# Kernel tuning notes

Hardware: AMD Instinct MI355X
Metric: run time of the kernel (lower is better)

## Reference

```python
import jax, jax.numpy as jnp
import numpy as np

# NOTE: submodules (VecLayerNorm, VecLinear, VecActivation, VNAttention,
# VNCrossAttention, VNDynamicGraphAttention) are not in the provided source;
# they are reconstructed per standard Vector-Neuron (VN) equivariant layers.

B, C, NQ, NV, K, HEADS = 2, 128, 2048, 2048, 16, 8
HID = 4 * C
EPS = 1e-6
NS = 0.2  # LeakyReLU(0.2) slope used by VecActivation


def vec_layernorm(x, gamma, beta):
    # x: [B,C,3,N] -- equivariant LN: normalize per-channel vector norms,
    # LayerNorm the norms over the channel dim, rescale directions.
    n = jnp.sqrt(jnp.sum(x * x, axis=2, keepdims=True) + EPS)  # [B,C,1,N]
    mu = jnp.mean(n, axis=1, keepdims=True)
    var = jnp.var(n, axis=1, keepdims=True)
    ln = (n - mu) / jnp.sqrt(var + EPS) * gamma[None, :, None, None] + beta[None, :, None, None]
    return x / (n + EPS) * ln


def vlin(x, W):
    # VecLinear: bias-free linear over channel dim (equivariance). x: [B,C,3,N]
    return jnp.einsum('oc,bctn->botn', W, x)


def vn_attention(xq, xkv, Wq, Wk, Wv, Wo):
    # Global equivariant multi-head attention; scores from 3D-vector inner products.
    Bq, Cc, _, Nq = xq.shape
    Dh = Cc // HEADS
    q = vlin(xq, Wq).reshape(Bq, HEADS, Dh, 3, Nq)
    k = vlin(xkv, Wk).reshape(Bq, HEADS, Dh, 3, -1)
    vv = vlin(xkv, Wv).reshape(Bq, HEADS, Dh, 3, -1)
    s = jnp.einsum('bhdtn,bhdtm->bhnm', q, k) / np.float32(np.sqrt(3 * Dh))
    a = jax.nn.softmax(s, axis=-1)
    o = jnp.einsum('bhnm,bhdtm->bhdtn', a, vv).reshape(Bq, Cc, 3, Nq)
    return vlin(o, Wo)


def graph_attention(xq, xv, idx, We):
    # Local kNN graph attention: gather neighbor features by idx, build edge
    # features concat(v_j - q_i, q_i) -> VecLinear, softmax-weight over k neighbors.
    Bq, Cc, _, Nq = xq.shape
    vt = jnp.transpose(xv, (0, 3, 2, 1))                 # [B,Nv,3,C]
    nbr = jax.vmap(lambda vb, ib: vb[ib])(vt, idx)       # [B,Nq,k,3,C]
    qt = jnp.transpose(xq, (0, 3, 2, 1))                 # [B,Nq,3,C]
    center = qt[:, :, None, :, :]
    edge = jnp.concatenate([nbr - center, jnp.broadcast_to(center, nbr.shape)], axis=-1)  # [B,Nq,k,3,2C]
    feat = jnp.einsum('oc,bnktc->bnkto', We, edge)        # [B,Nq,k,3,C]
    s = jnp.einsum('bntc,bnktc->bnk', qt, nbr) / np.float32(np.sqrt(3 * Cc))
    a = jax.nn.softmax(s, axis=-1)
    out = jnp.einsum('bnk,bnkto->bnto', a, feat)          # [B,Nq,3,C]
    return jnp.transpose(out, (0, 3, 2, 1))               # [B,C,3,Nq]


def vn_leaky(x, D):
    # VN-LeakyReLU: learned direction d = D x; reflect negative half-space.
    d = vlin(x, D)
    dot = jnp.sum(x * d, axis=2, keepdims=True)
    dsq = jnp.sum(d * d, axis=2, keepdims=True)
    xneg = x - (dot / (dsq + EPS)) * d
    return NS * x + (1.0 - NS) * jnp.where(dot >= 0, x, xneg)


def setup_inputs() -> dict:
    key = jax.random.key(0)
    ks = jax.random.split(key, 24)

    def w(k_, o, i):
        return jax.random.normal(k_, (o, i), jnp.float32) / np.float32(np.sqrt(i))

    inp = {
        'q': jax.random.normal(ks[0], (B, C, 3, NQ), jnp.float32),
        'v': jax.random.normal(ks[1], (B, C, 3, NV), jnp.float32),
        'q_pos': jax.random.normal(ks[2], (B, NQ, 3), jnp.float32),
        'v_pos': jax.random.normal(ks[3], (B, NV, 3), jnp.float32),
        'self_attn_idx': jax.random.randint(ks[4], (B, NQ, K), 0, NQ),
        'cross_attn_idx': jax.random.randint(ks[5], (B, NQ, K), 0, NV),
        # VecLayerNorm affine params (norm1, norm2, norm_q, norm_v)
        'g1': jnp.ones((C,), jnp.float32), 'b1': jnp.zeros((C,), jnp.float32),
        'g2': jnp.ones((C,), jnp.float32), 'b2': jnp.zeros((C,), jnp.float32),
        'gq': jnp.ones((C,), jnp.float32), 'bq': jnp.zeros((C,), jnp.float32),
        'gv': jnp.ones((C,), jnp.float32), 'bv': jnp.zeros((C,), jnp.float32),
        # self attention (global VN attn + local graph attn + concat merge)
        'Wq_s': w(ks[6], C, C), 'Wk_s': w(ks[7], C, C), 'Wv_s': w(ks[8], C, C), 'Wo_s': w(ks[9], C, C),
        'We_s': w(ks[10], C, 2 * C), 'Wm_s': w(ks[11], C, 2 * C),
        # cross attention
        'Wq_c': w(ks[12], C, C), 'Wk_c': w(ks[13], C, C), 'Wv_c': w(ks[14], C, C), 'Wo_c': w(ks[15], C, C),
        'We_c': w(ks[16], C, 2 * C), 'Wm_c': w(ks[17], C, 2 * C),
        # MLP: VecLinear(C->4C) -> VN-LeakyReLU -> VecLinear(4C->C)
        'W1': w(ks[18], HID, C), 'Dact': w(ks[19], HID, HID), 'W2': w(ks[20], C, HID),
    }
    return inp


def reference(q, v, q_pos, v_pos, self_attn_idx, cross_attn_idx,
              g1, b1, g2, b2, gq, bq, gv, bv,
              Wq_s, Wk_s, Wv_s, Wo_s, We_s, Wm_s,
              Wq_c, Wk_c, Wv_c, Wo_c, We_c, Wm_c,
              W1, Dact, W2):
    # --- self-attention block (norm1 -> global attn + kNN graph attn -> merge -> residual)
    nx = vec_layernorm(q, g1, b1)
    f1 = vn_attention(nx, nx, Wq_s, Wk_s, Wv_s, Wo_s)
    f2 = graph_attention(nx, nx, self_attn_idx, We_s)
    q = q + vlin(jnp.concatenate([f1, f2], axis=1), Wm_s)
    # --- cross-attention block (norm_q / norm_v -> global cross attn + kNN cross graph attn -> merge -> residual)
    nq = vec_layernorm(q, gq, bq)
    nv = vec_layernorm(v, gv, bv)
    f1 = vn_attention(nq, nv, Wq_c, Wk_c, Wv_c, Wo_c)
    f2 = graph_attention(nq, nv, cross_attn_idx, We_c)
    q = q + vlin(jnp.concatenate([f1, f2], axis=1), Wm_c)
    # --- equivariant MLP (norm2 -> VecLinear -> VN-LeakyReLU -> VecLinear -> residual)
    nx = vec_layernorm(q, g2, b2)
    h = vn_leaky(vlin(nx, W1), Dact)
    q = q + vlin(h, W2)
    return q
```

## Files before the change

kernel.cpp:

```cpp
#include <hip/hip_runtime.h>
#include <math.h>

#define B_    2
#define C_    128
#define N_    2048
#define HID_  512
#define HEADS_ 8
#define EPS_  1e-6f
#define NS_   0.2f
#define KSPLIT 8

typedef __attribute__((ext_vector_type(8))) short short8v;
typedef __attribute__((ext_vector_type(4))) float f32x4;
typedef unsigned short ush;
typedef unsigned int u32;

__device__ inline ush f2bf(float f) {
    unsigned u = __float_as_uint(f);
    u += 0x7FFF + ((u >> 16) & 1);
    return (ush)(u >> 16);
}
__device__ inline float bf2f(ush u) { return __uint_as_float((u32)u << 16); }

__device__ inline u32 splitpack(float x) {
    ush hi = f2bf(x);
    float hf = __uint_as_float((u32)hi << 16);
    ush lo = f2bf(x - hf);
    return ((u32)hi << 16) | (u32)lo;
}

__device__ inline void unpack_hi(const u32* buf, short8v& h0, short8v& h1) {
    ush h[16];
    #pragma unroll
    for (int j = 0; j < 16; ++j) h[j] = (ush)(buf[j] >> 16);
    h0 = *(short8v*)&h[0]; h1 = *(short8v*)&h[8];
}

struct LNArgs {
    const float* x[2]; const float* g[2]; const float* bt[2]; ush* ysp[2];
};
__global__ __launch_bounds__(256) void ln_kernel(LNArgs a)
{
    __shared__ float norms[128][32];
    __shared__ float red1[8][32];
    __shared__ float red2[8][32];
    const int s = blockIdx.z;
    const float* x = a.x[s];
    const float* gma = a.g[s];
    const float* bta = a.bt[s];
    ush* ysp = a.ysp[s];

    const int b  = blockIdx.y;
    const int n0 = blockIdx.x * 32;
    const int nn = threadIdx.x & 31;
    const int cg = threadIdx.x >> 5;

    float s1 = 0.f, s2 = 0.f;
    for (int it = 0; it < 16; ++it) {
        int c = it * 8 + cg;
        size_t base = ((size_t)(b * C_ + c) * 3) * N_ + n0 + nn;
        float x0 = x[base], x1 = x[base + N_], x2 = x[base + 2 * N_];
        float nr = sqrtf(x0 * x0 + x1 * x1 + x2 * x2 + EPS_);
        norms[c][nn] = nr;
        s1 += nr; s2 += nr * nr;
    }
    red1[cg][nn] = s1; red2[cg][nn] = s2;
    __syncthreads();
    float S1 = 0.f, S2 = 0.f;
    #pragma unroll
    for (int g = 0; g < 8; ++g) { S1 += red1[g][nn]; S2 += red2[g][nn]; }
    float mu   = S1 * (1.f / 128.f);
    float var  = S2 * (1.f / 128.f) - mu * mu;
    float rstd = rsqrtf(var + EPS_);

    for (int it = 0; it < 16; ++it) {
        int c = it * 8 + cg;
        float nr = norms[c][nn];
        float ln = (nr - mu) * rstd * gma[c] + bta[c];
        float sc = ln / (nr + EPS_);
        size_t base = ((size_t)(b * C_ + c) * 3) * N_ + n0 + nn;
        ysp[base]          = f2bf(x[base] * sc);
        ysp[base + N_]     = f2bf(x[base + N_] * sc);
        ysp[base + 2 * N_] = f2bf(x[base + 2 * N_] * sc);
    }
}

struct WCArgs { const float* src[9]; u32* dst[9]; int n[9]; float scale[9]; };
__global__ __launch_bounds__(256) void wconv_kernel(WCArgs a)
{
    const int w = blockIdx.y;
    const int i = blockIdx.x * 256 + threadIdx.x;
    if (i < a.n[w]) a.dst[w][i] = splitpack(a.src[w][i] * a.scale[w]);
}

struct WFArgs {
    const float* Wm[2]; const float* Wo[2]; const float* We[2];
    u32* Wfa[2]; u32* Wfb[2];
};
__global__ __launch_bounds__(256) void wfuse_kernel(WFArgs a)
{
    const int tg = blockIdx.x * 256 + threadIdx.x;
    const int p = tg / 49152;
    const int rem = tg % 49152;
    if (rem < 16384) {
        const int o = rem >> 7, k = rem & 127;
        const float* Wm = a.Wm[p];
        const float* Wo = a.Wo[p];
        float acc = 0.f;
        #pragma unroll 4
        for (int c = 0; c < 128; ++c)
            acc += Wm[o * 256 + c] * Wo[c * 128 + k];
        a.Wfa[p][o * 128 + k] = splitpack(acc);
    } else {
        const int r2 = rem - 16384;
        const int o = r2 >> 8, k = r2 & 255;
        const float* Wm = a.Wm[p];
        const float* We = a.We[p];
        float acc = 0.f;
        #pragma unroll 4
        for (int c = 0; c < 128; ++c)
            acc += Wm[o * 256 + 128 + c] * We[c * 256 + k];
        a.Wfb[p][o * 256 + k] = splitpack(acc);
    }
}

template <int XMODE, int OMODE, bool XBF>
__device__ __forceinline__ void gemm_tile(
    const u32* __restrict__ Wsp, int wstride,
    const void* __restrict__ Xv, int K,
    const float* __restrict__ Z, float* __restrict__ Y,
    ush* __restrict__ Ybf, ush* __restrict__ Ytr,
    int b, int m0, int o0loc, int oglob, int Ostr,
    ush (*Wh)[64], ush (*Xh)[64])
{
    const int M = 3 * N_;
    const int tid = threadIdx.x;
    const int lane = tid & 63, wv = tid >> 6;
    const int col = lane & 15, grp = lane >> 4;
    const int wo = wv >> 1, wm = wv & 1;

    f32x4 acc[2][2];
    #pragma unroll
    for (int i = 0; i < 2; ++i)
        #pragma unroll
        for (int j = 0; j < 2; ++j) { f32x4 z = {0.f,0.f,0.f,0.f}; acc[i][j] = z; }

    for (int kk = 0; kk < K; kk += 64) {
        {
            const int o = tid >> 2, kg = tid & 3;
            const u32* src = Wsp + (size_t)(o0loc + o) * wstride + kk + kg * 16;
            u32 buf[16];
            #pragma unroll
            for (int j = 0; j < 4; ++j) *(uint4*)&buf[j * 4] = *(const uint4*)(src + j * 4);
            const int s0 = ((kg * 2)     ^ (o & 7)) << 3;
            const int s1 = ((kg * 2 + 1) ^ (o & 7)) << 3;
            short8v h0, h1; unpack_hi(buf, h0, h1);
            *(short8v*)&Wh[o][s0] = h0; *(short8v*)&Wh[o][s1] = h1;
        }
        if (XMODE == 0) {
            const int m = lane, kq = wv;
            const int s0 = ((kq * 2)     ^ (m & 7)) << 3;
            const int s1 = ((kq * 2 + 1) ^ (m & 7)) << 3;
            if (XBF) {
                const ush* src = (const ush*)Xv + ((size_t)b * K + kk + kq * 16) * M + m0 + m;
                ush h[16];
                #pragma unroll
                for (int j = 0; j < 16; ++j) h[j] = src[(size_t)j * M];
                *(short8v*)&Xh[m][s0] = *(short8v*)&h[0];
                *(short8v*)&Xh[m][s1] = *(short8v*)&h[8];
            } else {
                const u32* src = (const u32*)Xv + ((size_t)b * K + kk + kq * 16) * M + m0 + m;
                u32 buf[16];
                #pragma unroll
                for (int j = 0; j < 16; ++j) buf[j] = src[(size_t)j * M];
                short8v h0, h1; unpack_hi(buf, h0, h1);
                *(short8v*)&Xh[m][s0] = h0; *(short8v*)&Xh[m][s1] = h1;
            }
        } else {
            const int m = tid >> 2, kg = tid & 3;
            const int mg = m0 + m;
            const int n = mg & (N_ - 1), t = mg >> 11;
            const int s0 = ((kg * 2)     ^ (m & 7)) << 3;
            const int s1 = ((kg * 2 + 1) ^ (m & 7)) << 3;
            const ush* src = (const ush*)Xv + ((size_t)(b * N_ + n) * 3 + t) * K + kk + kg * 16;
            ush h[16];
            *(uint4*)&h[0] = *(const uint4*)(src);
            *(uint4*)&h[8] = *(const uint4*)(src + 8);
            *(short8v*)&Xh[m][s0] = *(short8v*)&h[0];
            *(short8v*)&Xh[m][s1] = *(short8v*)&h[8];
        }
        __syncthreads();
        #pragma unroll
        for (int kc = 0; kc < 2; ++kc) {
            const int sk = ((kc * 4 + grp) ^ (col & 7)) << 3;
            short8v ah0 = *(const short8v*)&Wh[wo * 32 + col][sk];
            short8v ah1 = *(const short8v*)&Wh[wo * 32 + 16 + col][sk];
            short8v xh0 = *(const short8v*)&Xh[wm * 32 + col][sk];
            short8v xh1 = *(const short8v*)&Xh[wm * 32 + 16 + col][sk];
            acc[0][0] = __builtin_amdgcn_mfma_f32_16x16x32_bf16(ah0, xh0, acc[0][0], 0, 0, 0);
            acc[0][1] = __builtin_amdgcn_mfma_f32_16x16x32_bf16(ah0, xh1, acc[0][1], 0, 0, 0);
            acc[1][0] = __builtin_amdgcn_mfma_f32_16x16x32_bf16(ah1, xh0, acc[1][0], 0, 0, 0);
            acc[1][1] = __builtin_amdgcn_mfma_f32_16x16x32_bf16(ah1, xh1, acc[1][1], 0, 0, 0);
        }
        __syncthreads();
    }
    #pragma unroll
    for (int of = 0; of < 2; ++of) {
        #pragma unroll
        for (int r = 0; r < 4; ++r) {
            const int o = oglob + wo * 32 + of * 16 + grp * 4 + r;
            #pragma unroll
            for (int mf = 0; mf < 2; ++mf) {
                const int mloc = m0 + wm * 32 + mf * 16 + col;
                const size_t idx = ((size_t)b * Ostr + o) * M + mloc;
                float v = acc[of][mf][r];
                if (OMODE == 0) {
                    if (Z) v += Z[idx];
                    Y[idx] = v;
                }
                if (OMODE == 3) Ybf[idx] = f2bf(v);
                if (OMODE == 4) {
                    ush bv = f2bf(v);
                    const int t = mloc >> 11, n = mloc & (N_ - 1);
                    const int h = (o >> 4) & 7, cl = o & 15;
                    const int d = cl * 3 + t;
                    if (o >= 256) {
                        const int kt = n >> 6, hh = (n >> 5) & 1, db = d >> 4;
                        const size_t idx2 = ((size_t)(b * 8 + h) * 192
                                           + (kt * 2 + hh) * 3 + db) * 512
                                          + (((n >> 3) & 3) * 16 + (d & 15)) * 8 + (n & 7);
                        Ybf[idx2] = bv;
                    } else {
                        const int isK = (o >> 7) & 1;
                        const int qg = n >> 4, half = d >> 5;
                        const size_t idx2 = ((size_t)(isK * 16 + b * 8 + h) * 256
                                           + qg * 2 + half) * 512
                                          + (((d >> 3) & 3) * 16 + (n & 15)) * 8 + (d & 7);
                        Ytr[idx2] = bv;
                    }
                }
            }
        }
    }
}

template <int XMODE, int OMODE, bool XBF>
__global__ __launch_bounds__(256) void gemm_kernel2(
    const u32* __restrict__ Wsp, int wstride,
    const void* __restrict__ Xv,
    const float* __restrict__ Z,
    float* __restrict__ Y, ush* __restrict__ Ybf,
    int Ostr, int obase, int K)
{
    __shared__ __align__(16) ush Wh[64][64];
    __shared__ __align__(16) ush Xh[64][64];
    gemm_tile<XMODE, OMODE, XBF>(Wsp, wstride, Xv, K, Z, Y, Ybf, nullptr,
                            blockIdx.z, blockIdx.x * 64,
                            blockIdx.y * 64, obase + blockIdx.y * 64, Ostr,
                            Wh, Xh);
}

__global__ __launch_bounds__(256) void wm2_kernel(
    const u32* __restrict__ Wfa, const u32* __restrict__ Wfb,
    const ush* __restrict__ ao, const ush* __restrict__ gb,
    const float* __restrict__ Z, float* __restrict__ Y)
{
    __shared__ __align__(16) ush Wh[64][64];
    __shared__ __align__(16) ush Xh[64][64];
    const int M = 3 * N_;
    const int b = blockIdx.z;
    const int m0 = blockIdx.x * 64;
    const int o0 = blockIdx.y * 64;
    const int tid = threadIdx.x;
    const int lane = tid & 63, wv = tid >> 6;
    const int col = lane & 15, grp = lane >> 4;
    const int wo = wv >> 1, wm = wv & 1;

    f32x4 acc[2][2];
    #pragma unroll
    for (int i = 0; i < 2; ++i)
        #pragma unroll
        for (int j = 0; j < 2; ++j) { f32x4 z = {0.f,0.f,0.f,0.f}; acc[i][j] = z; }

    for (int kk = 0; kk < 128; kk += 64) {
        {
            const int o = tid >> 2, kg = tid & 3;
            const u32* src = Wfa + (size_t)(o0 + o) * 128 + kk + kg * 16;
            u32 buf[16];
            #pragma unroll
            for (int j = 0; j < 4; ++j) *(uint4*)&buf[j * 4] = *(const uint4*)(src + j * 4);
            const int s0 = ((kg * 2)     ^ (o & 7)) << 3;
            const int s1 = ((kg * 2 + 1) ^ (o & 7)) << 3;
            short8v h0, h1; unpack_hi(buf, h0, h1);
            *(short8v*)&Wh[o][s0] = h0; *(short8v*)&Wh[o][s1] = h1;
        }
        {
            const int m = lane, kq = wv;
            const int s0 = ((kq * 2)     ^ (m & 7)) << 3;
            const int s1 = ((kq * 2 + 1) ^ (m & 7)) << 3;
            const ush* src = ao + ((size_t)b * 128 + kk + kq * 16) * M + m0 + m;
            ush h[16];
            #pragma unroll
            for (int j = 0; j < 16; ++j) h[j] = src[(size_t)j * M];
            *(short8v*)&Xh[m][s0] = *(short8v*)&h[0];
            *(short8v*)&Xh[m][s1] = *(short8v*)&h[8];
        }
        __syncthreads();
        #pragma unroll
        for (int kc = 0; kc < 2; ++kc) {
            const int sk = ((kc * 4 + grp) ^ (col & 7)) << 3;
            short8v ah0 = *(const short8v*)&Wh[wo * 32 + col][sk];
            short8v ah1 = *(const short8v*)&Wh[wo * 32 + 16 + col][sk];
            short8v xh0 = *(const short8v*)&Xh[wm * 32 + col][sk];
            short8v xh1 = *(const short8v*)&Xh[wm * 32 + 16 + col][sk];
            acc[0][0] = __builtin_amdgcn_mfma_f32_16x16x32_bf16(ah0, xh0, acc[0][0], 0, 0, 0);
            acc[0][1] = __builtin_amdgcn_mfma_f32_16x16x32_bf16(ah0, xh1, acc[0][1], 0, 0, 0);
            acc[1][0] = __builtin_amdgcn_mfma_f32_16x16x32_bf16(ah1, xh0, acc[1][0], 0, 0, 0);
            acc[1][1] = __builtin_amdgcn_mfma_f32_16x16x32_bf16(ah1, xh1, acc[1][1], 0, 0, 0);
        }
        __syncthreads();
    }

    for (int kk = 0; kk < 256; kk += 64) {
        {
            const int o = tid >> 2, kg = tid & 3;
            const u32* src = Wfb + (size_t)(o0 + o) * 256 + kk + kg * 16;
            u32 buf[16];
            #pragma unroll
            for (int j = 0; j < 4; ++j) *(uint4*)&buf[j * 4] = *(const uint4*)(src + j * 4);
            const int s0 = ((kg * 2)     ^ (o & 7)) << 3;
            const int s1 = ((kg * 2 + 1) ^ (o & 7)) << 3;
            short8v h0, h1; unpack_hi(buf, h0, h1);
            *(short8v*)&Wh[o][s0] = h0; *(short8v*)&Wh[o][s1] = h1;
        }
        {
            const int m = tid >> 2, kg = tid & 3;
            const int mg = m0 + m;
            const int n = mg & (N_ - 1), t = mg >> 11;
            const int s0 = ((kg * 2)     ^ (m & 7)) << 3;
            const int s1 = ((kg * 2 + 1) ^ (m & 7)) << 3;
            const ush* src = gb + ((size_t)(b * N_ + n) * 3 + t) * 256 + kk + kg * 16;
            ush h[16];
            *(uint4*)&h[0] = *(const uint4*)(src);
            *(uint4*)&h[8] = *(const uint4*)(src + 8);
            *(short8v*)&Xh[m][s0] = *(short8v*)&h[0];
            *(short8v*)&Xh[m][s1] = *(short8v*)&h[8];
        }
        __syncthreads();
        #pragma unroll
        for (int kc = 0; kc < 2; ++kc) {
            const int sk = ((kc * 4 + grp) ^ (col & 7)) << 3;
            short8v ah0 = *(const short8v*)&Wh[wo * 32 + col][sk];
            short8v ah1 = *(const short8v*)&Wh[wo * 32 + 16 + col][sk];
            short8v xh0 = *(const short8v*)&Xh[wm * 32 + col][sk];
            short8v xh1 = *(const short8v*)&Xh[wm * 32 + 16 + col][sk];
            acc[0][0] = __builtin_amdgcn_mfma_f32_16x16x32_bf16(ah0, xh0, acc[0][0], 0, 0, 0);
            acc[0][1] = __builtin_amdgcn_mfma_f32_16x16x32_bf16(ah0, xh1, acc[0][1], 0, 0, 0);
            acc[1][0] = __builtin_amdgcn_mfma_f32_16x16x32_bf16(ah1, xh0, acc[1][0], 0, 0, 0);
            acc[1][1] = __builtin_amdgcn_mfma_f32_16x16x32_bf16(ah1, xh1, acc[1][1], 0, 0, 0);
        }
        __syncthreads();
    }

    #pragma unroll
    for (int of = 0; of < 2; ++of) {
        #pragma unroll
        for (int r = 0; r < 4; ++r) {
            const int o = o0 + wo * 32 + of * 16 + grp * 4 + r;
            #pragma unroll
            for (int mf = 0; mf < 2; ++mf) {
                const int mloc = m0 + wm * 32 + mf * 16 + col;
                const size_t idx = ((size_t)b * 128 + o) * M + mloc;
                Y[idx] = acc[of][mf][r] + Z[idx];
            }
        }
    }
}

struct QKVArgs {
    const u32* W0; const u32* W1; const u32* W2;
    const ush* X0; const ush* X1; const ush* X2;
};

__global__ __launch_bounds__(256) void qkv_tr_kernel(QKVArgs A,
        ush* __restrict__ vfm, ush* __restrict__ qktb,
        const ush* __restrict__ ts0, ush* __restrict__ td0,
        const ush* __restrict__ ts1, ush* __restrict__ td1)
{
    __shared__ __align__(16) ush Wh[64][64];
    __shared__ __align__(16) ush Xh[64][64];
    __shared__ ush ttile[32][34];
    const int bx = blockIdx.x;
    if (bx < 1152) {
        const int z = bx / 576, rem = bx % 576;
        const int y = rem / 96, x = rem % 96;
        const int wi = y >> 1;
        const u32* W = wi == 0 ? A.W0 : (wi == 1 ? A.W1 : A.W2);
        const ush* X = wi == 0 ? A.X0 : (wi == 1 ? A.X1 : A.X2);
        gemm_tile<0, 4, true>(W, 128, X, 128, nullptr, nullptr, vfm, qktb,
                        z, x * 64, (y & 1) * 64, y * 64, 384,
                        Wh, Xh);
    } else {
        int i = bx - 1152;
        const int which = i / 1536; i %= 1536;
        const ush* src = which ? ts1 : ts0;
        ush* dst = which ? td1 : td0;
        const int x = i & 63, y = (i >> 6) & 3, z = i >> 8;
        const int b = z / 3, t = z % 3;
        const int n0 = x * 32, c0 = y * 32;
        const int tx = threadIdx.x & 31, ty = threadIdx.x >> 5;
        #pragma unroll
        for (int p = 0; p < 4; ++p) {
            int c = c0 + ty + p * 8;
            ttile[ty + p * 8][tx] = src[((size_t)(b * C_ + c) * 3 + t) * N_ + n0 + tx];
        }
        __syncthreads();
        #pragma unroll
        for (int p = 0; p < 4; ++p) {
            int n = n0 + ty + p * 8;
            dst[((size_t)(b * N_ + n) * 3 + t) * C_ + c0 + tx] = ttile[tx][ty + p * 8];
        }
    }
}

__global__ __launch_bounds__(256) void attn_mfma_kernel(
    const ush* __restrict__ vfm, const ush* __restrict__ qktb,
    ush* __restrict__ pacc, float* __restrict__ pml)
{
    __shared__ __align__(16) ush Pl[4][2][16][64];

    const int flat = blockIdx.x;
    const int xcd  = flat & 7;
    const int slot = flat >> 3;
    const int gid  = xcd * 4 + (slot >> 6);
    const int q32  = slot & 63;
    const int bh   = gid & 15;
    const int zz   = gid >> 4;

    const int tid = threadIdx.x;
    const int lane = tid & 63, wv = tid >> 6;
    const int col = lane & 15, grp = lane >> 4;
    const int c7  = col & 7;
    const int kz  = zz * 4 + wv;
    const int ks0 = kz * (N_ / KSPLIT);

    const ush* Qpl = qktb + (size_t)bh * 131072;
    const ush* Kpl = qktb + (size_t)(16 + bh) * 131072;
    const ush* Vpl = vfm  + (size_t)bh * 98304;

    short8v qf[2][2];
    #pragma unroll
    for (int qi = 0; qi < 2; ++qi) {
        const int qg = q32 * 2 + qi;
        qf[qi][0] = *(const short8v*)(Qpl + ((size_t)qg * 2 + 0) * 512 + lane * 8);
        qf[qi][1] = *(const short8v*)(Qpl + ((size_t)qg * 2 + 1) * 512 + lane * 8);
    }

    f32x4 acc[2][3];
    #pragma unroll
    for (int qi = 0; qi < 2; ++qi)
        #pragma unroll
        for (int db = 0; db < 3; ++db) { f32x4 z = {0.f,0.f,0.f,0.f}; acc[qi][db] = z; }
    float m_i[2] = {0.f, 0.f};
    float l_l[2] = {0.f, 0.f};

    const int NT = (N_ / KSPLIT) / 64;
    for (int mt = 0; mt < NT; ++mt) {
        const int m0 = ks0 + mt * 64;

        short8v ka[4][2];
        #pragma unroll
        for (int kb = 0; kb < 4; ++kb) {
            const size_t kg = (m0 >> 4) + kb;
            ka[kb][0] = *(const short8v*)(Kpl + (kg * 2 + 0) * 512 + lane * 8);
            ka[kb][1] = *(const short8v*)(Kpl + (kg * 2 + 1) * 512 + lane * 8);
        }
        const int kt = m0 >> 6;
        short8v vf[2][3];
        #pragma unroll
        for (int hh = 0; hh < 2; ++hh)
            #pragma unroll
            for (int db = 0; db < 3; ++db)
                vf[hh][db] = *(const short8v*)(Vpl + (size_t)((kt * 2 + hh) * 3 + db) * 512 + lane * 8);

        f32x4 sf[2][4];
        __builtin_amdgcn_s_setprio(1);
        #pragma unroll
        for (int qi = 0; qi < 2; ++qi)
            #pragma unroll
            for (int kb = 0; kb < 4; ++kb) {
                f32x4 z = {0.f, 0.f, 0.f, 0.f};
                z = __builtin_amdgcn_mfma_f32_16x16x32_bf16(ka[kb][0], qf[qi][0], z, 0, 0, 0);
                z = __builtin_amdgcn_mfma_f32_16x16x32_bf16(ka[kb][1], qf[qi][1], z, 0, 0, 0);
                sf[qi][kb] = z;
            }
        __builtin_amdgcn_s_setprio(0);

        #pragma unroll
        for (int qi = 0; qi < 2; ++qi) {
            float psum = 0.f;
            #pragma unroll
            for (int kb = 0; kb < 4; ++kb) {
                float e0 = __expf(sf[qi][kb][0] - m_i[qi]);
                float e1 = __expf(sf[qi][kb][1] - m_i[qi]);
                float e2 = __expf(sf[qi][kb][2] - m_i[qi]);
                float e3 = __expf(sf[qi][kb][3] - m_i[qi]);
                psum += (e0 + e1) + (e2 + e3);
                u32 r0, r1;
                asm("v_cvt_pk_bf16_f32 %0, %1, %2" : "=v"(r0) : "v"(e0), "v"(e1));
                asm("v_cvt_pk_bf16_f32 %0, %1, %2" : "=v"(r1) : "v"(e2), "v"(e3));
                const int un = (4 * kb + grp) ^ (c7 << 1);
                uint2 pk2; pk2.x = r0; pk2.y = r1;
                *(uint2*)&Pl[wv][qi][col][un << 2] = pk2;
            }
            l_l[qi] += psum;
        }

        __builtin_amdgcn_s_setprio(1);
        #pragma unroll
        for (int qi = 0; qi < 2; ++qi)
            #pragma unroll
            for (int hh = 0; hh < 2; ++hh) {
                const int ur = (8 * hh + 2 * grp) ^ (c7 << 1);
                short8v pf = *(const short8v*)&Pl[wv][qi][col][ur << 2];
                #pragma unroll
                for (int db = 0; db < 3; ++db)
                    acc[qi][db] = __builtin_amdgcn_mfma_f32_16x16x32_bf16(vf[hh][db], pf, acc[qi][db], 0, 0, 0);
            }
        __builtin_amdgcn_s_setprio(0);

        #pragma unroll
        for (int qi = 0; qi < 2; ++qi) {
            float pmax = -1e30f;
            #pragma unroll
            for (int kb = 0; kb < 4; ++kb)
                #pragma unroll
                for (int r = 0; r < 4; ++r) pmax = fmaxf(pmax, sf[qi][kb][r]);
            pmax = fmaxf(pmax, __shfl_xor(pmax, 16, 64));
            pmax = fmaxf(pmax, __shfl_xor(pmax, 32, 64));
            if (!__all(pmax - m_i[qi] <= 8.0f)) {
                float mnew = fmaxf(m_i[qi], pmax);
                float sc = __expf(m_i[qi] - mnew);
                l_l[qi] *= sc;
                #pragma unroll
                for (int db = 0; db < 3; ++db) {
                    acc[qi][db][0] *= sc; acc[qi][db][1] *= sc;
                    acc[qi][db][2] *= sc; acc[qi][db][3] *= sc;
                }
                m_i[qi] = mnew;
            }
        }
    }

    const int ntile = q32 >> 1, qh = q32 & 1;
    const size_t pb = (size_t)(kz * 16 + bh) * 32 + ntile;
    #pragma unroll
    for (int qi = 0; qi < 2; ++qi) {
        float l = l_l[qi];
        l += __shfl_xor(l, 16, 64);
        l += __shfl_xor(l, 32, 64);
        const int q = qh * 32 + qi * 16 + col;
        #pragma unroll
        for (int db = 0; db < 3; ++db)
            #pragma unroll
            for (int r = 0; r < 4; ++r) {
                int d = db * 16 + grp * 4 + r;
                pacc[pb * 3072 + d * 64 + q] = f2bf(acc[qi][db][r]);
            }
        if (grp == 0) {
            pml[pb * 128 + q]      = m_i[qi];
            pml[pb * 128 + 64 + q] = l;
        }
    }
}

__global__ __launch_bounds__(256) void reduce_graph_kernel(
    const ush* __restrict__ pacc, const float* __restrict__ pml,
    ush* __restrict__ ao,
    const ush* __restrict__ tq, const ush* __restrict__ tv,
    const int* __restrict__ idx, ush* __restrict__ gbuf)
{
    __shared__ float centerf[384];
    __shared__ ush nbr_l[16][384];
    __shared__ float sd[16];
    __shared__ int nbr_i[16];
    const int tid = threadIdx.x;

    if (blockIdx.x < 512) {
        const int nt = blockIdx.x & 31, bh = blockIdx.x >> 5;
        const int b = bh >> 3, h = bh & 7;
        const int q = tid & 63, dg = tid >> 6;

        size_t pb[KSPLIT];
        float m[KSPLIT], l[KSPLIT];
        #pragma unroll
        for (int kz = 0; kz < KSPLIT; ++kz) {
            pb[kz] = (size_t)(kz * 16 + bh) * 32 + nt;
            m[kz] = pml[pb[kz] * 128 + q];
            l[kz] = pml[pb[kz] * 128 + 64 + q];
        }
        float ms = -1e30f;
        #pragma unroll
        for (int kz = 0; kz < KSPLIT; ++kz) ms = fmaxf(ms, m[kz]);
        float w[KSPLIT], ls = 0.f;
        #pragma unroll
        for (int kz = 0; kz < KSPLIT; ++kz) { w[kz] = __expf(m[kz] - ms); ls += l[kz] * w[kz]; }
        const float inv = 1.f / ls;

        const size_t hb = ((size_t)(b * C_ + h * 16)) * 3 * N_;
        #pragma unroll
        for (int j = 0; j < 12; ++j) {
            int d = dg * 12 + j;
            float o = 0.f;
            #pragma unroll
            for (int kz = 0; kz < KSPLIT; ++kz)
                o += bf2f(pacc[pb[kz] * 3072 + d * 64 + q]) * w[kz];
            ao[hb + (size_t)d * N_ + nt * 64 + q] = f2bf(o * inv);
        }
    } else {
        const int j = blockIdx.x - 512;
        const int b = j >> 11, n = j & 2047;
        const ush* qrow = tq + (size_t)(b * N_ + n) * 384;
        for (int e = tid; e < 384; e += 256) centerf[e] = bf2f(qrow[e]);
        if (tid < 16) nbr_i[tid] = idx[(size_t)(b * N_ + n) * 16 + tid];
        __syncthreads();

        const int lane = tid & 63, wv = tid >> 6;
        for (int kk = 0; kk < 4; ++kk) {
            int k = wv * 4 + kk;
            const u32* vrow = (const u32*)(tv + ((size_t)b * N_ + nbr_i[k]) * 384);
            float p = 0.f;
            #pragma unroll
            for (int jj = 0; jj < 3; ++jj) {
                int e2 = lane + jj * 64;
                u32 v2 = vrow[e2];
                ((u32*)nbr_l[k])[e2] = v2;
                p += centerf[e2 * 2]     * bf2f((ush)(v2 & 0xffff))
                   + centerf[e2 * 2 + 1] * bf2f((ush)(v2 >> 16));
            }
            #pragma unroll
            for (int off = 32; off; off >>= 1) p += __shfl_down(p, off, 64);
            if (lane == 0) sd[k] = p * 0.05103103630798288f;
        }
        __syncthreads();

        float mx = -1e30f;
        #pragma unroll
        for (int k = 0; k < 16; ++k) mx = fmaxf(mx, sd[k]);
        float a[16]; float ssum = 0.f;
        #pragma unroll
        for (int k = 0; k < 16; ++k) { a[k] = __expf(sd[k] - mx); ssum += a[k]; }
        float inv = 1.f / ssum;

        for (int e = tid; e < 384; e += 256) {
            float accv = 0.f;
            #pragma unroll
            for (int k = 0; k < 16; ++k)
                accv += a[k] * bf2f(nbr_l[k][e]);
            accv *= inv;
            float ce = centerf[e];
            int t = e >> 7, c = e & 127;
            size_t gb = ((size_t)(b * N_ + n) * 3 + t) * 256;
            gbuf[gb + c]       = f2bf(accv - ce);
            gbuf[gb + 128 + c] = f2bf(ce);
        }
    }
}

__global__ __launch_bounds__(256) void leaky_kernel(const ush* __restrict__ x,
                                                    const ush* __restrict__ d,
                                                    ush* __restrict__ y)
{
    size_t p = (size_t)blockIdx.x * 256 + threadIdx.x;
    size_t bh = p / N_, n = p % N_;
    size_t base = bh * 3 * N_ + n;
    float x0 = bf2f(x[base]), x1 = bf2f(x[base + N_]), x2 = bf2f(x[base + 2 * N_]);
    float d0 = bf2f(d[base]), d1 = bf2f(d[base + N_]), d2 = bf2f(d[base + 2 * N_]);
    float dot = x0 * d0 + x1 * d1 + x2 * d2;
    float dsq = d0 * d0 + d1 * d1 + d2 * d2;
    float f = dot / (dsq + EPS_);
    bool pos = dot >= 0.f;
    float y0 = pos ? x0 : x0 - f * d0;
    float y1 = pos ? x1 : x1 - f * d1;
    float y2 = pos ? x2 : x2 - f * d2;
    y[base]          = f2bf(NS_ * x0 + (1.f - NS_) * y0);
    y[base + N_]     = f2bf(NS_ * x1 + (1.f - NS_) * y1);
    y[base + 2 * N_] = f2bf(NS_ * x2 + (1.f - NS_) * y2);
}

extern "C" void kernel_launch(void* const* d_in, const int* in_sizes, int n_in,
                              void* d_out, int out_size, void* d_ws, size_t ws_size,
                              hipStream_t stream)
{
    const float* q_in = (const float*)d_in[0];
    const float* v_in = (const float*)d_in[1];
    const int*   idx_s = (const int*)d_in[4];
    const int*   idx_c = (const int*)d_in[5];
    const float* g1 = (const float*)d_in[6];
    const float* b1 = (const float*)d_in[7];
    const float* g2 = (const float*)d_in[8];
    const float* b2 = (const float*)d_in[9];
    const float* gq = (const float*)d_in[10];
    const float* bq = (const float*)d_in[11];
    const float* gv = (const float*)d_in[12];
    const float* bv = (const float*)d_in[13];
    float* out = (float*)d_out;
    float* ws  = (float*)d_ws;

    const size_t S1 = (size_t)B_ * C_ * 3 * N_;
    ush*   gbuf_b= (ush*)(ws);
    ush*   nx_b  = (ush*)(ws + 2*S1);
    ush*   nv_b  = (ush*)(ws + 3*S1);
    ush*   vfm   = (ush*)(ws + 4*S1);
    ush*   qktb  = (ush*)(ws + 5*S1) + S1;
    ush*   ao_b  = (ush*)(ws + 7*S1);
    float* qa    = ws + 12*S1;
    float* qb    = ws + 13*S1;
    ush*   t1_b  = (ush*)(ws + 14*S1);
    ush*   t2_b  = (ush*)(ws + 15*S1);
    u32*   wsp   = (u32*)(ws + 16*S1);
    ush*   pacc  = (ush*)(ws + 8*S1);
    float* pml   = (float*)(ws + 2*S1);
    ush*   hd_b  = (ush*)(ws + 1*S1);
    ush*   h1_b  = (ush*)(ws + 14*S1);
    ush*   h1_b2 = (ush*)(ws + 8*S1);

    const int wn[9]   = {16384,16384,16384, 16384,16384,16384, 65536,262144,65536};
    const int wsrc[9] = {14,15,16, 20,21,22, 26,27,28};
    u32* wd[9];
    {
        int off = 0;
        for (int i = 0; i < 9; ++i) { wd[i] = wsp + off; off += wn[i]; }
    }
    u32 *Wq_s = wd[0], *Wk_s = wd[1], *Wv_s = wd[2];
    u32 *Wq_c = wd[3], *Wk_c = wd[4], *Wv_c = wd[5];
    u32 *W1 = wd[6], *Dact = wd[7], *W2 = wd[8];
    u32* Wfa_s = wsp + 491520;
    u32* Wfb_s = Wfa_s + 16384;
    u32* Wfa_c = Wfb_s + 32768;
    u32* Wfb_c = Wfa_c + 16384;

    hipMemsetAsync(qktb, 0, (size_t)32 * 131072 * sizeof(ush), stream);

    {
        WCArgs a;
        for (int i = 0; i < 9; ++i) {
            a.src[i] = (const float*)d_in[wsrc[i]];
            a.dst[i] = wd[i];
            a.n[i]   = wn[i];
            a.scale[i] = 1.f;
        }
        a.scale[0] = 0.14433756729740643f;
        a.scale[3] = 0.14433756729740643f;
        wconv_kernel<<<dim3(1024, 9), 256, 0, stream>>>(a);
    }
    {
        WFArgs a;
        a.Wm[0] = (const float*)d_in[19]; a.Wo[0] = (const float*)d_in[17]; a.We[0] = (const float*)d_in[18];
        a.Wm[1] = (const float*)d_in[25]; a.Wo[1] = (const float*)d_in[23]; a.We[1] = (const float*)d_in[24];
        a.Wfa[0] = Wfa_s; a.Wfb[0] = Wfb_s;
        a.Wfa[1] = Wfa_c; a.Wfb[1] = Wfb_c;
        wfuse_kernel<<<dim3(384), 256, 0, stream>>>(a);
    }

    dim3 gwm(96, 2, B_);
    dim3 gg512(96, 8, B_);

    {
        LNArgs la{};
        la.x[0] = q_in; la.g[0] = g1; la.bt[0] = b1; la.ysp[0] = nx_b;
        ln_kernel<<<dim3(64, B_, 1), 256, 0, stream>>>(la);
    }
    {
        QKVArgs A{Wq_s, Wk_s, Wv_s, nx_b, nx_b, nx_b};
        qkv_tr_kernel<<<dim3(1152 + 1536), 256, 0, stream>>>(A, vfm, qktb, nx_b, t1_b, nullptr, nullptr);
    }
    attn_mfma_kernel<<<dim3(2048), 256, 0, stream>>>(vfm, qktb, pacc, pml);
    reduce_graph_kernel<<<dim3(512 + 4096), 256, 0, stream>>>(pacc, pml, ao_b, t1_b, t1_b, idx_s, gbuf_b);
    wm2_kernel<<<gwm, 256, 0, stream>>>(Wfa_s, Wfb_s, ao_b, gbuf_b, q_in, qa);

    {
        LNArgs la{};
        la.x[0] = qa;   la.g[0] = gq; la.bt[0] = bq; la.ysp[0] = nx_b;
        la.x[1] = v_in; la.g[1] = gv; la.bt[1] = bv; la.ysp[1] = nv_b;
        ln_kernel<<<dim3(64, B_, 2), 256, 0, stream>>>(la);
    }
    {
        QKVArgs A{Wq_c, Wk_c, Wv_c, nx_b, nv_b, nv_b};
        qkv_tr_kernel<<<dim3(1152 + 3072), 256, 0, stream>>>(A, vfm, qktb, nx_b, t1_b, nv_b, t2_b);
    }
    attn_mfma_kernel<<<dim3(2048), 256, 0, stream>>>(vfm, qktb, pacc, pml);
    reduce_graph_kernel<<<dim3(512 + 4096), 256, 0, stream>>>(pacc, pml, ao_b, t1_b, t2_b, idx_c, gbuf_b);
    wm2_kernel<<<gwm, 256, 0, stream>>>(Wfa_c, Wfb_c, ao_b, gbuf_b, qa, qb);

    {
        LNArgs la{};
        la.x[0] = qb; la.g[0] = g2; la.bt[0] = b2; la.ysp[0] = nx_b;
        ln_kernel<<<dim3(64, B_, 1), 256, 0, stream>>>(la);
    }
    gemm_kernel2<0,3,true><<<gg512, 256, 0, stream>>>(W1, 128, nx_b, nullptr, nullptr, h1_b, 512, 0, 128);
    gemm_kernel2<0,3,true><<<gg512, 256, 0, stream>>>(Dact, 512, h1_b, nullptr, nullptr, hd_b, 512, 0, 512);
    leaky_kernel<<<dim3((B_ * HID_ * N_) / 256), 256, 0, stream>>>(h1_b, hd_b, h1_b2);
    gemm_kernel2<0,0,true><<<dim3(96, 2, B_), 256, 0, stream>>>(W2, 512, h1_b2, qb, out, nullptr, 128, 0, 512);
}
```

Before: 239.2 us.

## Halve attention key split and merge weight setup kernels into one launch

The attention key dimension is now split into 4 chunks instead of 8, so each wave covers twice as many keys. The attention grid is halved and the block-to-(batch·head) mapping is simplified. This cuts the partial outputs written and later reduced, but leaves fewer blocks to occupy the GPU. Separately, the weight-conversion and weight-fusion kernels are merged into one launch to save launch overhead.

```diff
diff --git a/kernel.cpp b/kernel.cpp
--- a/kernel.cpp
+++ b/kernel.cpp
@@ -8,7 +8,7 @@
 #define HEADS_ 8
 #define EPS_  1e-6f
 #define NS_   0.2f
-#define KSPLIT 8
+#define KSPLIT 4
 
 typedef __attribute__((ext_vector_type(8))) short short8v;
 typedef __attribute__((ext_vector_type(4))) float f32x4;
@@ -85,42 +85,42 @@
     }
 }
 
-struct WCArgs { const float* src[9]; u32* dst[9]; int n[9]; float scale[9]; };
-__global__ __launch_bounds__(256) void wconv_kernel(WCArgs a)
-{
-    const int w = blockIdx.y;
-    const int i = blockIdx.x * 256 + threadIdx.x;
-    if (i < a.n[w]) a.dst[w][i] = splitpack(a.src[w][i] * a.scale[w]);
-}
-
-struct WFArgs {
+struct SetupArgs {
+    const float* src[9]; u32* dst[9]; int n[9]; float scale[9];
     const float* Wm[2]; const float* Wo[2]; const float* We[2];
     u32* Wfa[2]; u32* Wfb[2];
 };
-__global__ __launch_bounds__(256) void wfuse_kernel(WFArgs a)
-{
-    const int tg = blockIdx.x * 256 + threadIdx.x;
-    const int p = tg / 49152;
-    const int rem = tg % 49152;
-    if (rem < 16384) {
-        const int o = rem >> 7, k = rem & 127;
-        const float* Wm = a.Wm[p];
-        const float* Wo = a.Wo[p];
-        float acc = 0.f;
-        #pragma unroll 4
-        for (int c = 0; c < 128; ++c)
-            acc += Wm[o * 256 + c] * Wo[c * 128 + k];
-        a.Wfa[p][o * 128 + k] = splitpack(acc);
+__global__ __launch_bounds__(256) void setup_kernel(SetupArgs a)
+{
+    const int bx = blockIdx.x;
+    if (bx < 9216) {
+        const int w = bx / 1024;
+        const int i = (bx % 1024) * 256 + threadIdx.x;
+        if (i < a.n[w]) a.dst[w][i] = splitpack(a.src[w][i] * a.scale[w]);
     } else {
-        const int r2 = rem - 16384;
-        const int o = r2 >> 8, k = r2 & 255;
-        const float* Wm = a.Wm[p];
-        const float* We = a.We[p];
-        float acc = 0.f;
-        #pragma unroll 4
-        for (int c = 0; c < 128; ++c)
-            acc += Wm[o * 256 + 128 + c] * We[c * 256 + k];
-        a.Wfb[p][o * 256 + k] = splitpack(acc);
+        const int tg = (bx - 9216) * 256 + threadIdx.x;
+        const int p = tg / 49152;
+        const int rem = tg % 49152;
+        if (rem < 16384) {
+            const int o = rem >> 7, k = rem & 127;
+            const float* Wm = a.Wm[p];
+            const float* Wo = a.Wo[p];
+            float acc = 0.f;
+            #pragma unroll 4
+            for (int c = 0; c < 128; ++c)
+                acc += Wm[o * 256 + c] * Wo[c * 128 + k];
+            a.Wfa[p][o * 128 + k] = splitpack(acc);
+        } else {
+            const int r2 = rem - 16384;
+            const int o = r2 >> 8, k = r2 & 255;
+            const float* Wm = a.Wm[p];
+            const float* We = a.We[p];
+            float acc = 0.f;
+            #pragma unroll 4
+            for (int c = 0; c < 128; ++c)
+                acc += Wm[o * 256 + 128 + c] * We[c * 256 + k];
+            a.Wfb[p][o * 256 + k] = splitpack(acc);
+        }
     }
 }
 
@@ -432,16 +432,14 @@
     const int flat = blockIdx.x;
     const int xcd  = flat & 7;
     const int slot = flat >> 3;
-    const int gid  = xcd * 4 + (slot >> 6);
+    const int bh   = xcd * 2 + (slot >> 6);
     const int q32  = slot & 63;
-    const int bh   = gid & 15;
-    const int zz   = gid >> 4;
 
     const int tid = threadIdx.x;
     const int lane = tid & 63, wv = tid >> 6;
     const int col = lane & 15, grp = lane >> 4;
     const int c7  = col & 7;
-    const int kz  = zz * 4 + wv;
+    const int kz  = wv;
     const int ks0 = kz * (N_ / KSPLIT);
 
     const ush* Qpl = qktb + (size_t)bh * 131072;
@@ -743,7 +741,7 @@
     hipMemsetAsync(qktb, 0, (size_t)32 * 131072 * sizeof(ush), stream);
 
     {
-        WCArgs a;
+        SetupArgs a{};
         for (int i = 0; i < 9; ++i) {
             a.src[i] = (const float*)d_in[wsrc[i]];
             a.dst[i] = wd[i];
@@ -752,15 +750,11 @@
         }
         a.scale[0] = 0.14433756729740643f;
         a.scale[3] = 0.14433756729740643f;
-        wconv_kernel<<<dim3(1024, 9), 256, 0, stream>>>(a);
-    }
-    {
-        WFArgs a;
         a.Wm[0] = (const float*)d_in[19]; a.Wo[0] = (const float*)d_in[17]; a.We[0] = (const float*)d_in[18];
         a.Wm[1] = (const float*)d_in[25]; a.Wo[1] = (const float*)d_in[23]; a.We[1] = (const float*)d_in[24];
         a.Wfa[0] = Wfa_s; a.Wfb[0] = Wfb_s;
         a.Wfa[1] = Wfa_c; a.Wfb[1] = Wfb_c;
-        wfuse_kernel<<<dim3(384), 256, 0, stream>>>(a);
+        setup_kernel<<<dim3(9216 + 384), 256, 0, stream>>>(a);
     }
 
     dim3 gwm(96, 2, B_);
@@ -775,7 +769,7 @@
         QKVArgs A{Wq_s, Wk_s, Wv_s, nx_b, nx_b, nx_b};
         qkv_tr_kernel<<<dim3(1152 + 1536), 256, 0, stream>>>(A, vfm, qktb, nx_b, t1_b, nullptr, nullptr);
     }
-    attn_mfma_kernel<<<dim3(2048), 256, 0, stream>>>(vfm, qktb, pacc, pml);
+    attn_mfma_kernel<<<dim3(1024), 256, 0, stream>>>(vfm, qktb, pacc, pml);
     reduce_graph_kernel<<<dim3(512 + 4096), 256, 0, stream>>>(pacc, pml, ao_b, t1_b, t1_b, idx_s, gbuf_b);
     wm2_kernel<<<gwm, 256, 0, stream>>>(Wfa_s, Wfb_s, ao_b, gbuf_b, q_in, qa);
 
@@ -789,7 +783,7 @@
         QKVArgs A{Wq_c, Wk_c, Wv_c, nx_b, nv_b, nv_b};
         qkv_tr_kernel<<<dim3(1152 + 3072), 256, 0, stream>>>(A, vfm, qktb, nx_b, t1_b, nv_b, t2_b);
     }
-    attn_mfma_kernel<<<dim3(2048), 256, 0, stream>>>(vfm, qktb, pacc, pml);
+    attn_mfma_kernel<<<dim3(1024), 256, 0, stream>>>(vfm, qktb, pacc, pml);
     reduce_graph_kernel<<<dim3(512 + 4096), 256, 0, stream>>>(pacc, pml, ao_b, t1_b, t2_b, idx_c, gbuf_b);
     wm2_kernel<<<gwm, 256, 0, stream>>>(Wfa_c, Wfb_c, ao_b, gbuf_b, qa, qb);
 
```

Result: faster. 231.5 us (-3.2%).
